# Kernel tuning notes

Hardware: AMD Instinct MI355X
Metric: run time of the kernel (lower is better)

The kernel has to match this reference:

```python
import jax, jax.numpy as jnp
import numpy as np

DIM = 128       # pair channel dim
HID = 128       # orign_dim (projection dim)
N = 384         # sequence length (square pair map)
B = 1
EPS = 1e-5


def layer_norm(x, w, b):
    m = jnp.mean(x, axis=-1, keepdims=True)
    v = jnp.mean(jnp.square(x - m), axis=-1, keepdims=True)
    return (x - m) * jax.lax.rsqrt(v + EPS) * w + b


def setup_inputs() -> dict:
    key = jax.random.key(0)
    ks = jax.random.split(key, 16)
    s = 0.02
    return {
        "x": jax.random.normal(ks[0], (B, N, N, DIM), jnp.float32),
        "norm_w": jnp.ones((DIM,), jnp.float32),
        "norm_b": jnp.zeros((DIM,), jnp.float32),
        "left_w": jax.random.normal(ks[1], (HID, DIM), jnp.float32) * s,
        "left_b": jnp.zeros((HID,), jnp.float32),
        "right_w": jax.random.normal(ks[2], (HID, DIM), jnp.float32) * s,
        "right_b": jnp.zeros((HID,), jnp.float32),
        # gates: module inits weight=0, bias=1; use small random weights + bias 1
        # to keep the same math while exercising nontrivial values
        "lgate_w": jax.random.normal(ks[3], (HID, DIM), jnp.float32) * s,
        "lgate_b": jnp.ones((HID,), jnp.float32),
        "rgate_w": jax.random.normal(ks[4], (HID, DIM), jnp.float32) * s,
        "rgate_b": jnp.ones((HID,), jnp.float32),
        "ogate_w": jax.random.normal(ks[5], (HID, DIM), jnp.float32) * s,
        "ogate_b": jnp.ones((HID,), jnp.float32),
        "ton_w": jnp.ones((HID,), jnp.float32),
        "ton_b": jnp.zeros((HID,), jnp.float32),
        "out_w": jax.random.normal(ks[6], (DIM, HID), jnp.float32) * s,
        "out_b": jnp.zeros((DIM,), jnp.float32),
    }


def reference(x, norm_w, norm_b, left_w, left_b, right_w, right_b,
              lgate_w, lgate_b, rgate_w, rgate_b, ogate_w, ogate_b,
              ton_w, ton_b, out_w, out_b):
    xn = layer_norm(x, norm_w, norm_b)                       # [B,N,N,D]
    lin = lambda w, b: jnp.einsum('bijd,ed->bije', xn, w) + b
    left = lin(left_w, left_b) * jax.nn.sigmoid(lin(lgate_w, lgate_b))
    right = lin(right_w, right_b) * jax.nn.sigmoid(lin(rgate_w, rgate_b))
    out_gate = jax.nn.sigmoid(lin(ogate_w, ogate_b))
    # ingoing mix: '... k j d, ... k i d -> ... i j d'
    out = jnp.einsum('bkjd,bkid->bijd', left, right)         # [B,N,N,H]
    out = layer_norm(out, ton_w, ton_b)
    out = jnp.einsum('bijh,dh->bijd', out, out_w) + out_b
    return out * out_gate
```

## Files before the change

### kernel.cpp

```cpp
#include <hip/hip_runtime.h>
#include <stdint.h>

typedef unsigned short u16;
typedef short bf16x8 __attribute__((ext_vector_type(8)));
typedef short bf16x4 __attribute__((ext_vector_type(4)));
typedef float f32x4 __attribute__((ext_vector_type(4)));

#define NN 384
#define DIMC 128
#define NPOS (NN*NN)
#define EPSV 1e-5f
#define LNS 136

__device__ __forceinline__ u16 f2b(float f){
  union { float f; uint32_t u; } v; v.f = f;
  return (u16)((v.u + 0x7FFFu + ((v.u >> 16) & 1u)) >> 16);
}
__device__ __forceinline__ float b2f(u16 h){
  union { uint32_t u; float f; } v; v.u = ((uint32_t)h) << 16;
  return v.f;
}
__device__ __forceinline__ float sigm(float z){ return 1.0f/(1.0f + __expf(-z)); }

__device__ __forceinline__ void glds16(const u16* g, u16* l){
  __builtin_amdgcn_global_load_lds((const __attribute__((address_space(1))) void*)(g),
                                   (__attribute__((address_space(3))) void*)(l), 16, 0, 0);
}

__global__ void wconv_k(const float* __restrict__ s0, const float* __restrict__ s1,
                        const float* __restrict__ s2, const float* __restrict__ s3,
                        const float* __restrict__ s4, const float* __restrict__ s5,
                        u16* __restrict__ dst){
  int bid = blockIdx.x;
  int m = bid >> 6;
  int off = ((bid & 63) << 8) + threadIdx.x;
  const float* src = s0;
  if (m==1) src=s1; else if (m==2) src=s2; else if (m==3) src=s3;
  else if (m==4) src=s4; else if (m==5) src=s5;
  dst[(m<<14) + off] = f2b(src[off]);
}

__global__ __launch_bounds__(256) void proj_k(
    const float* __restrict__ x, const float* __restrict__ nw, const float* __restrict__ nb,
    const u16* __restrict__ wb,
    const float* __restrict__ left_b, const float* __restrict__ lgate_b,
    const float* __restrict__ right_b, const float* __restrict__ rgate_b,
    const float* __restrict__ ogate_b,
    u16* __restrict__ Lp, u16* __restrict__ Rp, u16* __restrict__ gate)
{
  __shared__ u16 xn[64*LNS];
  __shared__ u16 trans[9216];
  const int tid = threadIdx.x, lane = tid & 63, wid = tid >> 6;
  const int bid = blockIdx.x;
  const int c = bid % NN, r0 = (bid / NN) * 64;

  float2 nw2 = *(const float2*)(nw + 2*lane);
  float2 nb2 = *(const float2*)(nb + 2*lane);
  float2 xv[16];
  #pragma unroll
  for (int t = 0; t < 16; ++t){
    int p = wid*16 + t;
    xv[t] = *(const float2*)(x + ((size_t)(r0 + p)*NN + c)*DIMC + 2*lane);
  }
  #pragma unroll
  for (int t = 0; t < 16; ++t){
    int p = wid*16 + t;
    float s = xv[t].x + xv[t].y, sq = xv[t].x*xv[t].x + xv[t].y*xv[t].y;
    #pragma unroll
    for (int o = 32; o; o >>= 1){ s += __shfl_xor(s, o); sq += __shfl_xor(sq, o); }
    float mean = s * (1.0f/128.0f);
    float var  = sq * (1.0f/128.0f) - mean*mean;
    float inv  = rsqrtf(var + EPSV);
    u16 h0 = f2b((xv[t].x - mean)*inv*nw2.x + nb2.x);
    u16 h1 = f2b((xv[t].y - mean)*inv*nw2.y + nb2.y);
    uint32_t pk = (uint32_t)h0 | ((uint32_t)h1 << 16);
    *(uint32_t*)(xn + p*LNS + 2*lane) = pk;
  }
  __syncthreads();

  const int l15 = lane & 15, lg = lane >> 4;
  const int kofs = lg * 8;
  const int wrow = (wid*32 + l15) * 128;
  const int xrowbase = l15 * LNS;

  #pragma unroll
  for (int pr = 0; pr < 2; ++pr){
    const u16* wV = wb + (pr*2 + 0)*16384;
    const u16* wG = wb + (pr*2 + 1)*16384;
    const float* bV = pr ? right_b : left_b;
    const float* bG = pr ? rgate_b : lgate_b;
    u16* dst = pr ? Rp : Lp;

    f32x4 aV[2][4], aG[2][4];
    #pragma unroll
    for (int n = 0; n < 2; ++n)
      #pragma unroll
      for (int pt = 0; pt < 4; ++pt){ aV[n][pt] = {0.f,0.f,0.f,0.f}; aG[n][pt] = {0.f,0.f,0.f,0.f}; }

    #pragma unroll
    for (int ks = 0; ks < 4; ++ks){
      bf16x8 xf[4];
      #pragma unroll
      for (int pt = 0; pt < 4; ++pt)
        xf[pt] = *(const bf16x8*)(xn + xrowbase + pt*16*LNS + ks*32 + kofs);
      #pragma unroll
      for (int n = 0; n < 2; ++n){
        bf16x8 wv = *(const bf16x8*)(wV + wrow + n*16*128 + ks*32 + kofs);
        bf16x8 wg = *(const bf16x8*)(wG + wrow + n*16*128 + ks*32 + kofs);
        #pragma unroll
        for (int pt = 0; pt < 4; ++pt){
          aV[n][pt] = __builtin_amdgcn_mfma_f32_16x16x32_bf16(wv, xf[pt], aV[n][pt], 0, 0, 0);
          aG[n][pt] = __builtin_amdgcn_mfma_f32_16x16x32_bf16(wg, xf[pt], aG[n][pt], 0, 0, 0);
        }
      }
    }
    #pragma unroll
    for (int n = 0; n < 2; ++n){
      int ebase = wid*32 + n*16 + lg*4;
      float4 bv4 = *(const float4*)(bV + ebase);
      float4 bg4 = *(const float4*)(bG + ebase);
      #pragma unroll
      for (int pt = 0; pt < 4; ++pt){
        #pragma unroll
        for (int r = 0; r < 4; ++r){
          float bv = r==0?bv4.x : r==1?bv4.y : r==2?bv4.z : bv4.w;
          float bg = r==0?bg4.x : r==1?bg4.y : r==2?bg4.z : bg4.w;
          float v = (aV[n][pt][r] + bv) * sigm(aG[n][pt][r] + bg);
          trans[(ebase + r)*72 + pt*16 + l15] = f2b(v);
        }
      }
    }
    __syncthreads();
    #pragma unroll
    for (int it = 0; it < 4; ++it){
      int idx = tid + it*256;
      int e = idx >> 3, s = idx & 7;
      *(bf16x8*)(dst + (size_t)e*NPOS + (size_t)c*NN + r0 + s*8) = *(const bf16x8*)(trans + e*72 + s*8);
    }
    __syncthreads();
  }

  {
    const u16* wO = wb + 4*16384;
    f32x4 aO[4][2];
    #pragma unroll
    for (int pt = 0; pt < 4; ++pt)
      #pragma unroll
      for (int n = 0; n < 2; ++n) aO[pt][n] = {0.f,0.f,0.f,0.f};

    #pragma unroll
    for (int ks = 0; ks < 4; ++ks){
      bf16x8 xf[4];
      #pragma unroll
      for (int pt = 0; pt < 4; ++pt)
        xf[pt] = *(const bf16x8*)(xn + xrowbase + pt*16*LNS + ks*32 + kofs);
      #pragma unroll
      for (int n = 0; n < 2; ++n){
        bf16x8 wo = *(const bf16x8*)(wO + wrow + n*16*128 + ks*32 + kofs);
        #pragma unroll
        for (int pt = 0; pt < 4; ++pt)
          aO[pt][n] = __builtin_amdgcn_mfma_f32_16x16x32_bf16(xf[pt], wo, aO[pt][n], 0, 0, 0);
      }
    }
    float bo0 = ogate_b[wid*32 + l15];
    float bo1 = ogate_b[wid*32 + 16 + l15];
    #pragma unroll
    for (int pt = 0; pt < 4; ++pt){
      #pragma unroll
      for (int n = 0; n < 2; ++n){
        int e = wid*32 + n*16 + l15;
        float bo = n ? bo1 : bo0;
        #pragma unroll
        for (int r = 0; r < 4; ++r){
          int p = pt*16 + lg*4 + r;
          trans[p*136 + e] = f2b(sigm(aO[pt][n][r] + bo));
        }
      }
    }
    __syncthreads();
    #pragma unroll
    for (int it = 0; it < 4; ++it){
      int idx = tid + it*256;
      int p = idx >> 4, s = idx & 15;
      *(bf16x8*)(gate + ((size_t)(r0 + p)*NN + c)*DIMC + s*8) = *(const bf16x8*)(trans + p*136 + s*8);
    }
  }
}

__global__ __launch_bounds__(256) void phase2_k(const u16* __restrict__ Rp, const u16* __restrict__ Lp,
                                                u16* __restrict__ outp){
  __shared__ u16 lds[17408];
  u16* At = lds;
  u16* Bt = lds + 8192;
  const int tid = threadIdx.x, lane = tid & 63, wid = tid >> 6;
  const int bid = blockIdx.x;
  const int d = bid / 9, tile = bid % 9;
  const int i0 = (tile/3)*128, j0 = (tile%3)*128;
  const u16* Rb = Rp + (size_t)d*NPOS;
  const u16* Lb = Lp + (size_t)d*NPOS;
  const int wm = wid >> 1, wn = wid & 1;
  const int iw = wm*64, jw = wn*64;
  const int l15 = lane & 15, lg = lane >> 4;
  const int rmask = l15 & 7;

  int srcoff[4];
  #pragma unroll
  for (int c = 0; c < 4; ++c){
    int idx = wid*256 + c*64 + lane;
    int row = idx >> 3, slot = idx & 7;
    srcoff[c] = row*NN + ((slot ^ (row & 7)) * 8);
  }

  f32x4 acc[4][4];
  #pragma unroll
  for (int m = 0; m < 4; ++m)
    #pragma unroll
    for (int n = 0; n < 4; ++n) acc[m][n] = {0.f,0.f,0.f,0.f};

  const u16* Rt0 = Rb + (size_t)i0*NN;
  const u16* Lt0 = Lb + (size_t)j0*NN;

  for (int k0 = 0; k0 < NN; k0 += 64){
    __syncthreads();
    #pragma unroll
    for (int c = 0; c < 4; ++c){
      glds16(Rt0 + k0 + srcoff[c], At + (wid*4 + c)*512);
      glds16(Lt0 + k0 + srcoff[c], Bt + (wid*4 + c)*512);
    }
    asm volatile("s_waitcnt vmcnt(0)" ::: "memory");
    __syncthreads();
    #pragma unroll
    for (int ks = 0; ks < 2; ++ks){
      int sl = ((ks*4 + lg) ^ rmask) * 8;
      bf16x8 af[4], bfr[4];
      #pragma unroll
      for (int m = 0; m < 4; ++m)
        af[m] = *(const bf16x8*)(At + (iw + m*16 + l15)*64 + sl);
      #pragma unroll
      for (int n = 0; n < 4; ++n)
        bfr[n] = *(const bf16x8*)(Bt + (jw + n*16 + l15)*64 + sl);
      #pragma unroll
      for (int m = 0; m < 4; ++m)
        #pragma unroll
        for (int n = 0; n < 4; ++n)
          acc[m][n] = __builtin_amdgcn_mfma_f32_16x16x32_bf16(af[m], bfr[n], acc[m][n], 0, 0, 0);
    }
  }

  __syncthreads();
  #pragma unroll
  for (int m = 0; m < 4; ++m)
    #pragma unroll
    for (int n = 0; n < 4; ++n)
      #pragma unroll
      for (int r = 0; r < 4; ++r)
        lds[(iw + m*16 + lg*4 + r)*136 + jw + n*16 + l15] = f2b(acc[m][n][r]);
  __syncthreads();
  u16* ob = outp + (size_t)d*NPOS;
  #pragma unroll
  for (int it = 0; it < 8; ++it){
    int idx = tid + it*256;
    int i = idx >> 4, s = idx & 15;
    *(bf16x8*)(ob + (size_t)(i0 + i)*NN + j0 + s*8) = *(const bf16x8*)(lds + i*136 + s*8);
  }
}

__global__ __launch_bounds__(256) void phase3_k(const u16* __restrict__ outp,
    const float* __restrict__ tonw, const float* __restrict__ tonb,
    const u16* __restrict__ wOut, const float* __restrict__ out_b,
    const u16* __restrict__ gate, float* __restrict__ out)
{
  __shared__ u16 xn2[64*132];
  __shared__ float reds[4][64], redq[4][64];
  __shared__ float marr[64], iarr[64];
  const int tid = threadIdx.x, lane = tid & 63, wid = tid >> 6;
  const int bid = blockIdx.x;
  const int i = bid % NN, j0 = (bid / NN) * 64;

  float rv[32];
  float s = 0.f, sq = 0.f;
  #pragma unroll
  for (int q = 0; q < 32; ++q){
    int h = wid*32 + q;
    float v = b2f(outp[(size_t)h*NPOS + (size_t)i*NN + j0 + lane]);
    rv[q] = v; s += v; sq += v*v;
  }
  reds[wid][lane] = s; redq[wid][lane] = sq;
  __syncthreads();
  if (tid < 64){
    float ts = reds[0][tid] + reds[1][tid] + reds[2][tid] + reds[3][tid];
    float tq = redq[0][tid] + redq[1][tid] + redq[2][tid] + redq[3][tid];
    float m  = ts * (1.f/128.f);
    float var = tq * (1.f/128.f) - m*m;
    marr[tid] = m; iarr[tid] = rsqrtf(var + EPSV);
  }
  __syncthreads();
  float m = marr[lane], inv = iarr[lane];
  #pragma unroll
  for (int q = 0; q < 32; ++q){
    int h = wid*32 + q;
    float v = (rv[q] - m)*inv*tonw[h] + tonb[h];
    xn2[lane*132 + h] = f2b(v);
  }
  __syncthreads();

  f32x4 acc[8];
  #pragma unroll
  for (int n = 0; n < 8; ++n) acc[n] = {0.f,0.f,0.f,0.f};
  const int row = wid*16 + (lane & 15);
  const int kofs = (lane >> 4) * 8;
  #pragma unroll
  for (int ks = 0; ks < 4; ++ks){
    const u16* ap = xn2 + row*132 + ks*32 + kofs;
    bf16x4 a0 = *(const bf16x4*)ap;
    bf16x4 a1 = *(const bf16x4*)(ap + 4);
    bf16x8 af = __builtin_shufflevector(a0, a1, 0,1,2,3,4,5,6,7);
    #pragma unroll
    for (int n = 0; n < 8; ++n){
      bf16x8 bm = *(const bf16x8*)(wOut + (n*16 + (lane & 15))*128 + ks*32 + kofs);
      acc[n] = __builtin_amdgcn_mfma_f32_16x16x32_bf16(af, bm, acc[n], 0, 0, 0);
    }
  }
  #pragma unroll
  for (int n = 0; n < 8; ++n){
    int dd = n*16 + (lane & 15);
    float bo = out_b[dd];
    #pragma unroll
    for (int r = 0; r < 4; ++r){
      int p = wid*16 + ((lane >> 4) << 2) + r;
      size_t base = ((size_t)i*NN + j0 + p)*DIMC + dd;
      float g = b2f(gate[base]);
      out[base] = (acc[n][r] + bo) * g;
    }
  }
}

extern "C" void kernel_launch(void* const* d_in, const int* in_sizes, int n_in,
                              void* d_out, int out_size, void* d_ws, size_t ws_size,
                              hipStream_t stream){
  const float* x       = (const float*)d_in[0];
  const float* norm_w  = (const float*)d_in[1];
  const float* norm_b  = (const float*)d_in[2];
  const float* left_w  = (const float*)d_in[3];
  const float* left_b  = (const float*)d_in[4];
  const float* right_w = (const float*)d_in[5];
  const float* right_b = (const float*)d_in[6];
  const float* lgate_w = (const float*)d_in[7];
  const float* lgate_b = (const float*)d_in[8];
  const float* rgate_w = (const float*)d_in[9];
  const float* rgate_b = (const float*)d_in[10];
  const float* ogate_w = (const float*)d_in[11];
  const float* ogate_b = (const float*)d_in[12];
  const float* ton_w   = (const float*)d_in[13];
  const float* ton_b   = (const float*)d_in[14];
  const float* out_w   = (const float*)d_in[15];
  const float* out_b   = (const float*)d_in[16];

  char* ws = (char*)d_ws;
  const size_t SZ = (size_t)NPOS * DIMC * sizeof(u16);
  u16* Lp   = (u16*)(ws);
  u16* Rp   = (u16*)(ws + SZ);
  u16* gate = (u16*)(ws + 2*SZ);
  u16* outp = (u16*)(ws + 3*SZ);
  u16* wb   = (u16*)(ws + 4*SZ);

  wconv_k<<<dim3(384), dim3(256), 0, stream>>>(left_w, lgate_w, right_w, rgate_w, ogate_w, out_w, wb);
  proj_k<<<dim3(2304), dim3(256), 0, stream>>>(x, norm_w, norm_b, wb,
      left_b, lgate_b, right_b, rgate_b, ogate_b, Lp, Rp, gate);
  phase2_k<<<dim3(1152), dim3(256), 0, stream>>>(Rp, Lp, outp);
  phase3_k<<<dim3(2304), dim3(256), 0, stream>>>(outp, ton_w, ton_b, wb + 5*16384, out_b, gate, (float*)d_out);
}
```

Before: 194.7 us.

## Drop LDS transpose staging in projection kernel and write outputs directly

The projection kernel now stores the L/R projections and the output gate straight from MFMA accumulators to global memory as 2-byte scattered stores, removing the shared-memory transpose buffer and its barriers. The gate layout changes to channel-major [d][col][row], and phase3 reads it with the matching strided index. The LayerNorm prologue loads 8 floats per lane and reduces across 16 lanes, and the sigmoid uses a hardware reciprocal. The cost is narrow uncoalesced global stores, plus strided 2-byte gate reads in phase3, in exchange for less LDS traffic and more occupancy.

```diff
diff --git a/kernel.cpp b/kernel.cpp
--- a/kernel.cpp
+++ b/kernel.cpp
@@ -20,7 +20,9 @@
   union { uint32_t u; float f; } v; v.u = ((uint32_t)h) << 16;
   return v.f;
 }
-__device__ __forceinline__ float sigm(float z){ return 1.0f/(1.0f + __expf(-z)); }
+__device__ __forceinline__ float sigm(float z){
+  return __builtin_amdgcn_rcpf(1.0f + __expf(-z));
+}
 
 __device__ __forceinline__ void glds16(const u16* g, u16* l){
   __builtin_amdgcn_global_load_lds((const __attribute__((address_space(1))) void*)(g),
@@ -49,36 +51,44 @@
     u16* __restrict__ Lp, u16* __restrict__ Rp, u16* __restrict__ gate)
 {
   __shared__ u16 xn[64*LNS];
-  __shared__ u16 trans[9216];
   const int tid = threadIdx.x, lane = tid & 63, wid = tid >> 6;
   const int bid = blockIdx.x;
   const int c = bid % NN, r0 = (bid / NN) * 64;
-
-  float2 nw2 = *(const float2*)(nw + 2*lane);
-  float2 nb2 = *(const float2*)(nb + 2*lane);
-  float2 xv[16];
-  #pragma unroll
-  for (int t = 0; t < 16; ++t){
-    int p = wid*16 + t;
-    xv[t] = *(const float2*)(x + ((size_t)(r0 + p)*NN + c)*DIMC + 2*lane);
-  }
-  #pragma unroll
-  for (int t = 0; t < 16; ++t){
-    int p = wid*16 + t;
-    float s = xv[t].x + xv[t].y, sq = xv[t].x*xv[t].x + xv[t].y*xv[t].y;
-    #pragma unroll
-    for (int o = 32; o; o >>= 1){ s += __shfl_xor(s, o); sq += __shfl_xor(sq, o); }
-    float mean = s * (1.0f/128.0f);
-    float var  = sq * (1.0f/128.0f) - mean*mean;
-    float inv  = rsqrtf(var + EPSV);
-    u16 h0 = f2b((xv[t].x - mean)*inv*nw2.x + nb2.x);
-    u16 h1 = f2b((xv[t].y - mean)*inv*nw2.y + nb2.y);
-    uint32_t pk = (uint32_t)h0 | ((uint32_t)h1 << 16);
-    *(uint32_t*)(xn + p*LNS + 2*lane) = pk;
-  }
-  __syncthreads();
-
   const int l15 = lane & 15, lg = lane >> 4;
+
+  {
+    float4 w0 = *(const float4*)(nw + l15*8);
+    float4 w1 = *(const float4*)(nw + l15*8 + 4);
+    float4 bb0 = *(const float4*)(nb + l15*8);
+    float4 bb1 = *(const float4*)(nb + l15*8 + 4);
+    #pragma unroll
+    for (int it = 0; it < 4; ++it){
+      int p = wid*16 + it*4 + lg;
+      const float* xp = x + ((size_t)(r0 + p)*NN + c)*DIMC + l15*8;
+      float4 v0 = *(const float4*)xp;
+      float4 v1 = *(const float4*)(xp + 4);
+      float s  = (v0.x+v0.y)+(v0.z+v0.w)+((v1.x+v1.y)+(v1.z+v1.w));
+      float sq = v0.x*v0.x+v0.y*v0.y+v0.z*v0.z+v0.w*v0.w
+               + v1.x*v1.x+v1.y*v1.y+v1.z*v1.z+v1.w*v1.w;
+      #pragma unroll
+      for (int o = 8; o; o >>= 1){ s += __shfl_xor(s, o); sq += __shfl_xor(sq, o); }
+      float mean = s * (1.0f/128.0f);
+      float var  = sq * (1.0f/128.0f) - mean*mean;
+      float inv  = rsqrtf(var + EPSV);
+      bf16x8 o8;
+      o8[0] = (short)f2b((v0.x - mean)*inv*w0.x + bb0.x);
+      o8[1] = (short)f2b((v0.y - mean)*inv*w0.y + bb0.y);
+      o8[2] = (short)f2b((v0.z - mean)*inv*w0.z + bb0.z);
+      o8[3] = (short)f2b((v0.w - mean)*inv*w0.w + bb0.w);
+      o8[4] = (short)f2b((v1.x - mean)*inv*w1.x + bb1.x);
+      o8[5] = (short)f2b((v1.y - mean)*inv*w1.y + bb1.y);
+      o8[6] = (short)f2b((v1.z - mean)*inv*w1.z + bb1.z);
+      o8[7] = (short)f2b((v1.w - mean)*inv*w1.w + bb1.w);
+      *(bf16x8*)(xn + p*LNS + l15*8) = o8;
+    }
+  }
+  __syncthreads();
+
   const int kofs = lg * 8;
   const int wrow = (wid*32 + l15) * 128;
   const int xrowbase = l15 * LNS;
@@ -120,33 +130,26 @@
       float4 bv4 = *(const float4*)(bV + ebase);
       float4 bg4 = *(const float4*)(bG + ebase);
       #pragma unroll
-      for (int pt = 0; pt < 4; ++pt){
-        #pragma unroll
-        for (int r = 0; r < 4; ++r){
-          float bv = r==0?bv4.x : r==1?bv4.y : r==2?bv4.z : bv4.w;
-          float bg = r==0?bg4.x : r==1?bg4.y : r==2?bg4.z : bg4.w;
+      for (int r = 0; r < 4; ++r){
+        float bv = r==0?bv4.x : r==1?bv4.y : r==2?bv4.z : bv4.w;
+        float bg = r==0?bg4.x : r==1?bg4.y : r==2?bg4.z : bg4.w;
+        u16* base = dst + (size_t)(ebase + r)*NPOS + (size_t)c*NN + r0 + l15;
+        #pragma unroll
+        for (int pt = 0; pt < 4; ++pt){
           float v = (aV[n][pt][r] + bv) * sigm(aG[n][pt][r] + bg);
-          trans[(ebase + r)*72 + pt*16 + l15] = f2b(v);
+          base[pt*16] = f2b(v);
         }
       }
     }
-    __syncthreads();
-    #pragma unroll
-    for (int it = 0; it < 4; ++it){
-      int idx = tid + it*256;
-      int e = idx >> 3, s = idx & 7;
-      *(bf16x8*)(dst + (size_t)e*NPOS + (size_t)c*NN + r0 + s*8) = *(const bf16x8*)(trans + e*72 + s*8);
-    }
-    __syncthreads();
   }
 
   {
     const u16* wO = wb + 4*16384;
-    f32x4 aO[4][2];
-    #pragma unroll
-    for (int pt = 0; pt < 4; ++pt)
-      #pragma unroll
-      for (int n = 0; n < 2; ++n) aO[pt][n] = {0.f,0.f,0.f,0.f};
+    f32x4 aO[2][4];
+    #pragma unroll
+    for (int n = 0; n < 2; ++n)
+      #pragma unroll
+      for (int pt = 0; pt < 4; ++pt) aO[n][pt] = {0.f,0.f,0.f,0.f};
 
     #pragma unroll
     for (int ks = 0; ks < 4; ++ks){
@@ -159,30 +162,21 @@
         bf16x8 wo = *(const bf16x8*)(wO + wrow + n*16*128 + ks*32 + kofs);
         #pragma unroll
         for (int pt = 0; pt < 4; ++pt)
-          aO[pt][n] = __builtin_amdgcn_mfma_f32_16x16x32_bf16(xf[pt], wo, aO[pt][n], 0, 0, 0);
+          aO[n][pt] = __builtin_amdgcn_mfma_f32_16x16x32_bf16(wo, xf[pt], aO[n][pt], 0, 0, 0);
       }
     }
-    float bo0 = ogate_b[wid*32 + l15];
-    float bo1 = ogate_b[wid*32 + 16 + l15];
-    #pragma unroll
-    for (int pt = 0; pt < 4; ++pt){
-      #pragma unroll
-      for (int n = 0; n < 2; ++n){
-        int e = wid*32 + n*16 + l15;
-        float bo = n ? bo1 : bo0;
-        #pragma unroll
-        for (int r = 0; r < 4; ++r){
-          int p = pt*16 + lg*4 + r;
-          trans[p*136 + e] = f2b(sigm(aO[pt][n][r] + bo));
-        }
+    #pragma unroll
+    for (int n = 0; n < 2; ++n){
+      int ebase = wid*32 + n*16 + lg*4;
+      float4 bo4 = *(const float4*)(ogate_b + ebase);
+      #pragma unroll
+      for (int r = 0; r < 4; ++r){
+        float bo = r==0?bo4.x : r==1?bo4.y : r==2?bo4.z : bo4.w;
+        u16* base = gate + (size_t)(ebase + r)*NPOS + (size_t)c*NN + r0 + l15;
+        #pragma unroll
+        for (int pt = 0; pt < 4; ++pt)
+          base[pt*16] = f2b(sigm(aO[n][pt][r] + bo));
       }
-    }
-    __syncthreads();
-    #pragma unroll
-    for (int it = 0; it < 4; ++it){
-      int idx = tid + it*256;
-      int p = idx >> 4, s = idx & 15;
-      *(bf16x8*)(gate + ((size_t)(r0 + p)*NN + c)*DIMC + s*8) = *(const bf16x8*)(trans + p*136 + s*8);
     }
   }
 }
@@ -276,6 +270,7 @@
   const int tid = threadIdx.x, lane = tid & 63, wid = tid >> 6;
   const int bid = blockIdx.x;
   const int i = bid % NN, j0 = (bid / NN) * 64;
+  const int l15 = lane & 15, lg = lane >> 4;
 
   float rv[32];
   float s = 0.f, sq = 0.f;
@@ -307,8 +302,8 @@
   f32x4 acc[8];
   #pragma unroll
   for (int n = 0; n < 8; ++n) acc[n] = {0.f,0.f,0.f,0.f};
-  const int row = wid*16 + (lane & 15);
-  const int kofs = (lane >> 4) * 8;
+  const int row = wid*16 + l15;
+  const int kofs = lg * 8;
   #pragma unroll
   for (int ks = 0; ks < 4; ++ks){
     const u16* ap = xn2 + row*132 + ks*32 + kofs;
@@ -317,19 +312,19 @@
     bf16x8 af = __builtin_shufflevector(a0, a1, 0,1,2,3,4,5,6,7);
     #pragma unroll
     for (int n = 0; n < 8; ++n){
-      bf16x8 bm = *(const bf16x8*)(wOut + (n*16 + (lane & 15))*128 + ks*32 + kofs);
+      bf16x8 bm = *(const bf16x8*)(wOut + (n*16 + l15)*128 + ks*32 + kofs);
       acc[n] = __builtin_amdgcn_mfma_f32_16x16x32_bf16(af, bm, acc[n], 0, 0, 0);
     }
   }
   #pragma unroll
   for (int n = 0; n < 8; ++n){
-    int dd = n*16 + (lane & 15);
+    int dd = n*16 + l15;
     float bo = out_b[dd];
     #pragma unroll
     for (int r = 0; r < 4; ++r){
-      int p = wid*16 + ((lane >> 4) << 2) + r;
+      int p = wid*16 + lg*4 + r;
+      float g = b2f(gate[(size_t)dd*NPOS + (size_t)(j0 + p)*NN + i]);
       size_t base = ((size_t)i*NN + j0 + p)*DIMC + dd;
-      float g = b2f(gate[base]);
       out[base] = (acc[n][r] + bo) * g;
     }
   }
```

Result: slower. 255.7 us (+31.4%).
